# Performance work log

Measured on AMD Instinct MI355X. Metric: run time of the kernel, lower is better.

## Reference

```python
import jax, jax.numpy as jnp
import numpy as np

B, N, ND = 4096, 28, 3        # batch, nodes (2 hands x 14 joints), xyz
ED, DD = 512, 256             # encoder dim, decoder dim
H, DH = 8, 64                 # heads, dim_head (inner = 512)
EDEPTH, DDEPTH = 2, 1
EMLP, DMLP = 4 * ED, 4 * DD
NM = 14                       # num_masked = int(0.5 * 28)


def _ln(x, s, b):
    m = jnp.mean(x, -1, keepdims=True)
    v = jnp.var(x, -1, keepdims=True)
    return (x - m) * jax.lax.rsqrt(v + 1e-5) * s + b


def _transformer(x, a, ln1_s, ln1_b, Wqkv, Wo, bo, ln2_s, ln2_b, W1, b1, W2, b2):
    # pre-norm transformer; adjacency a [b,n,n] enters as an additive attention bias
    b, n, _ = x.shape
    scale = DH ** -0.5
    for i in range(ln1_s.shape[0]):
        h = _ln(x, ln1_s[i], ln1_b[i])
        q, k, v = jnp.split(h @ Wqkv[i], 3, axis=-1)
        q = q.reshape(b, n, H, DH).transpose(0, 2, 1, 3)
        k = k.reshape(b, n, H, DH).transpose(0, 2, 1, 3)
        v = v.reshape(b, n, H, DH).transpose(0, 2, 1, 3)
        dots = jnp.einsum('bhid,bhjd->bhij', q, k) * scale + a[:, None]
        attn = jax.nn.softmax(dots, axis=-1)
        o = jnp.einsum('bhij,bhjd->bhid', attn, v).transpose(0, 2, 1, 3).reshape(b, n, H * DH)
        x = x + o @ Wo[i] + bo[i]
        h2 = _ln(x, ln2_s[i], ln2_b[i])
        x = x + jax.nn.gelu(h2 @ W1[i] + b1[i]) @ W2[i] + b2[i]
    return x


def setup_inputs() -> dict:
    key = jax.random.key(0)
    ks = iter(jax.random.split(key, 40))
    nrm = lambda shp, s=0.02: jax.random.normal(next(ks), shp, dtype=jnp.float32) * s
    x = jax.random.normal(next(ks), (B, N, ND), dtype=jnp.float32)
    a = jax.random.uniform(next(ks), (B, N, N), dtype=jnp.float32)
    perm = jnp.argsort(jax.random.uniform(next(ks), (B, N)), axis=-1).astype(jnp.int32)
    masked_indices, unmasked_indices = perm[:, :NM], perm[:, NM:]
    inp = dict(x=x, a=a, masked_indices=masked_indices, unmasked_indices=unmasked_indices)
    inp.update(
        W_emb=nrm((ND, ED)), b_emb=jnp.zeros((ED,), jnp.float32), pos_emb=nrm((N, ED), 0.02),
        e_ln1_s=jnp.ones((EDEPTH, ED)), e_ln1_b=jnp.zeros((EDEPTH, ED)),
        e_Wqkv=nrm((EDEPTH, ED, 3 * H * DH)), e_Wo=nrm((EDEPTH, H * DH, ED)), e_bo=jnp.zeros((EDEPTH, ED)),
        e_ln2_s=jnp.ones((EDEPTH, ED)), e_ln2_b=jnp.zeros((EDEPTH, ED)),
        e_W1=nrm((EDEPTH, ED, EMLP)), e_b1=jnp.zeros((EDEPTH, EMLP)),
        e_W2=nrm((EDEPTH, EMLP, ED)), e_b2=jnp.zeros((EDEPTH, ED)),
        enc2dec_W=nrm((ED, DD)), enc2dec_b=jnp.zeros((DD,), jnp.float32),
        mask_token=nrm((DD,), 1.0), dec_pos_emb=nrm((N, DD), 0.02),
        d_ln1_s=jnp.ones((DDEPTH, DD)), d_ln1_b=jnp.zeros((DDEPTH, DD)),
        d_Wqkv=nrm((DDEPTH, DD, 3 * H * DH)), d_Wo=nrm((DDEPTH, H * DH, DD)), d_bo=jnp.zeros((DDEPTH, DD)),
        d_ln2_s=jnp.ones((DDEPTH, DD)), d_ln2_b=jnp.zeros((DDEPTH, DD)),
        d_W1=nrm((DDEPTH, DD, DMLP)), d_b1=jnp.zeros((DDEPTH, DMLP)),
        d_W2=nrm((DDEPTH, DMLP, DD)), d_b2=jnp.zeros((DDEPTH, DD)),
        pred_W=nrm((DD, ND)), pred_b=jnp.zeros((ND,), jnp.float32),
    )
    return inp


def reference(x, a, masked_indices, unmasked_indices,
              W_emb, b_emb, pos_emb,
              e_ln1_s, e_ln1_b, e_Wqkv, e_Wo, e_bo, e_ln2_s, e_ln2_b, e_W1, e_b1, e_W2, e_b2,
              enc2dec_W, enc2dec_b, mask_token, dec_pos_emb,
              d_ln1_s, d_ln1_b, d_Wqkv, d_Wo, d_bo, d_ln2_s, d_ln2_b, d_W1, d_b1, d_W2, d_b2,
              pred_W, pred_b):
    # node embedding (1x1 conv over nodes == per-node linear) + positional embedding
    tokens = x @ W_emb + b_emb + pos_emb                                   # [B,N,ED]
    unm_tok = jnp.take_along_axis(tokens, unmasked_indices[:, :, None], axis=1)  # [B,N-NM,ED]
    masked_nodes = jnp.take_along_axis(x, masked_indices[:, :, None], axis=1)    # [B,NM,ND]
    # batched adjacency slicing (replaces the per-sample python loop in torch)
    unmasked_a = jax.vmap(lambda ai, ii: ai[ii[:, None], ii[None, :]])(a, unmasked_indices)
    enc = _transformer(unm_tok, unmasked_a,
                       e_ln1_s, e_ln1_b, e_Wqkv, e_Wo, e_bo, e_ln2_s, e_ln2_b, e_W1, e_b1, e_W2, e_b2)
    dec_tok = enc @ enc2dec_W + enc2dec_b                                  # [B,N-NM,DD]
    mask_toks = mask_token + dec_pos_emb[masked_indices]                   # [B,NM,DD]
    # NOTE: faithful to original: unmasked pos-emb tokens are computed but NOT used in the cat
    decoder_tokens = jnp.concatenate([mask_toks, dec_tok], axis=1)         # [B,N,DD]
    decoded = _transformer(decoder_tokens, a,
                           d_ln1_s, d_ln1_b, d_Wqkv, d_Wo, d_bo, d_ln2_s, d_ln2_b, d_W1, d_b1, d_W2, d_b2)
    mt = jnp.take_along_axis(decoded, masked_indices[:, :, None], axis=1)  # [B,NM,DD]
    masked_pred = mt @ pred_W + pred_b                                     # [B,NM,ND]
    recon_loss = jnp.mean((masked_pred - masked_nodes) ** 2)
    return (decoder_tokens, masked_nodes, masked_indices, masked_pred, recon_loss)
```

## Files before the change

### kernel.cpp

```cpp
#include <hip/hip_runtime.h>
#include <math.h>

#define B_TOT 4096
#define N_SEQ 28
#define NDIM 3
#define ED 512
#define DD 256
#define NH 8
#define DHD 64
#define EMLP 2048
#define DMLP 1024
#define NM 14
#define NU 14

typedef __attribute__((ext_vector_type(8))) short short8;
typedef __attribute__((ext_vector_type(4))) float f32x4;
typedef unsigned short ushort_t;
typedef unsigned int uint_t;

__device__ __forceinline__ float gelu_f(float x) {
    float t = 0.7978845608028654f * (x + 0.044715f * x * x * x);
    float e = __expf(2.0f * t);
    float th = 1.0f - 2.0f / (e + 1.0f);
    return 0.5f * x * (1.0f + th);
}
__device__ __forceinline__ ushort_t f2bf(float f) {
    union { float f; uint_t u; } c; c.f = f;
    uint_t u = c.u;
    return (ushort_t)((u + 0x7FFFu + ((u >> 16) & 1u)) >> 16);
}
__device__ __forceinline__ float bf2f(ushort_t h) {
    union { uint_t u; float f; } c; c.u = ((uint_t)h) << 16;
    return c.f;
}
__device__ __forceinline__ float bf_lo(uint_t u) {
    union { uint_t u; float f; } c; c.u = u << 16;
    return c.f;
}
__device__ __forceinline__ float bf_hi(uint_t u) {
    union { uint_t u; float f; } c; c.u = u & 0xFFFF0000u;
    return c.f;
}
__device__ __forceinline__ void gl_lds16(const ushort_t* g, ushort_t* l) {
    __builtin_amdgcn_global_load_lds(
        (const __attribute__((address_space(1))) unsigned int*)g,
        (__attribute__((address_space(3))) unsigned int*)l, 16, 0, 0);
}

__global__ void k_zero(float* p) { p[threadIdx.x] = 0.0f; }
__global__ void k_final(const float* acc, float* out) {
    out[0] = acc[0] * (1.0f / (float)(B_TOT * NM * NDIM));
}

__global__ void k_wconv(const float* __restrict__ W, ushort_t* __restrict__ Wt, int K, int N) {
    __shared__ float tile[32][33];
    int n0 = blockIdx.x * 32, k0 = blockIdx.y * 32;
    int tr = threadIdx.x >> 5, tc = threadIdx.x & 31;
#pragma unroll
    for (int i = 0; i < 4; ++i)
        tile[tr + i * 8][tc] = W[(size_t)(k0 + tr + i * 8) * N + n0 + tc];
    __syncthreads();
#pragma unroll
    for (int i = 0; i < 4; ++i)
        Wt[(size_t)(n0 + tr + i * 8) * K + k0 + tc] = f2bf(tile[tc][tr + i * 8]);
}

__global__ void k_embed(const float* __restrict__ x, const float* __restrict__ a,
                        const int* __restrict__ mi, const int* __restrict__ ui,
                        const float* __restrict__ W_emb, const float* __restrict__ b_emb,
                        const float* __restrict__ pos_emb,
                        ushort_t* __restrict__ X, float* __restrict__ ua,
                        float* __restrict__ out_mn, float* __restrict__ out_midx,
                        int base) {
    int s = blockIdx.x;
    int g = base + s;
    int t = threadIdx.x;
    for (int i = 0; i < NU; ++i) {
        int u = ui[g * NU + i];
        float x0 = x[((size_t)g * N_SEQ + u) * NDIM + 0];
        float x1 = x[((size_t)g * N_SEQ + u) * NDIM + 1];
        float x2 = x[((size_t)g * N_SEQ + u) * NDIM + 2];
        for (int d = t; d < ED; d += 256) {
            X[((size_t)s * NU + i) * ED + d] = f2bf(
                x0 * W_emb[d] + x1 * W_emb[ED + d] + x2 * W_emb[2 * ED + d]
                + b_emb[d] + pos_emb[(size_t)u * ED + d]);
        }
    }
    for (int idx = t; idx < NU * NU; idx += 256) {
        int i = idx / NU, j = idx % NU;
        int uii = ui[g * NU + i], ujj = ui[g * NU + j];
        ua[(size_t)s * NU * NU + idx] = a[(size_t)g * N_SEQ * N_SEQ + (size_t)uii * N_SEQ + ujj];
    }
    for (int idx = t; idx < NM * NDIM; idx += 256) {
        int i = idx / NDIM, c = idx % NDIM;
        int m = mi[g * NM + i];
        out_mn[((size_t)g * NM + i) * NDIM + c] = x[((size_t)g * N_SEQ + m) * NDIM + c];
    }
    for (int i = t; i < NM; i += 256) {
        out_midx[(size_t)g * NM + i] = (float)mi[g * NM + i];
    }
}

template <int D>
__global__ void k_ln(const ushort_t* __restrict__ in, ushort_t* __restrict__ out,
                     const float* __restrict__ sc, const float* __restrict__ bi, int M) {
    int wave = threadIdx.x >> 6;
    int lane = threadIdx.x & 63;
    int row = blockIdx.x * 4 + wave;
    if (row >= M) return;
    constexpr int PL = D / 64;
    const ushort_t* rp = in + (size_t)row * D + lane * PL;
    uint_t u[PL / 2];
    if (PL == 8) *(uint4*)u = *(const uint4*)rp;
    else *(uint2*)u = *(const uint2*)rp;
    float v[PL];
    float sum = 0.f, sq = 0.f;
#pragma unroll
    for (int q = 0; q < PL / 2; ++q) {
        v[2 * q] = bf_lo(u[q]);
        v[2 * q + 1] = bf_hi(u[q]);
    }
#pragma unroll
    for (int j = 0; j < PL; ++j) { sum += v[j]; sq += v[j] * v[j]; }
#pragma unroll
    for (int o = 32; o >= 1; o >>= 1) {
        sum += __shfl_xor(sum, o);
        sq += __shfl_xor(sq, o);
    }
    float mean = sum * (1.0f / D);
    float var = sq * (1.0f / D) - mean * mean;
    float r = rsqrtf(var + 1e-5f);
    uint_t w[PL / 2];
#pragma unroll
    for (int q = 0; q < PL / 2; ++q) {
        int d = lane * PL + 2 * q;
        float a0 = (v[2 * q] - mean) * r * sc[d] + bi[d];
        float a1 = (v[2 * q + 1] - mean) * r * sc[d + 1] + bi[d + 1];
        w[q] = (uint_t)f2bf(a0) | ((uint_t)f2bf(a1) << 16);
    }
    ushort_t* op = out + (size_t)row * D + lane * PL;
    if (PL == 8) *(uint4*)op = *(uint4*)w;
    else *(uint2*)op = *(uint2*)w;
}

template <int ACT>
__global__ __launch_bounds__(256) void k_gemm_mfma(
    const ushort_t* __restrict__ A, const ushort_t* __restrict__ Wt,
    const float* __restrict__ bias, const ushort_t* __restrict__ res,
    ushort_t* __restrict__ Cout, int M, int N, int K) {
    __shared__ __align__(16) ushort_t smem[17408];
    ushort_t* As0 = smem;
    ushort_t* As1 = smem + 4096;
    ushort_t* Bs0 = smem + 8192;
    ushort_t* Bs1 = smem + 12288;

    const int t = threadIdx.x;
    const int gx = gridDim.x;
    int flat = blockIdx.y * gx + blockIdx.x;
    int nwg = gx * gridDim.y;
    int q8 = nwg >> 3, r8 = nwg & 7;
    int xcd = flat & 7, loc = flat >> 3;
    int wg = (xcd < r8 ? xcd * (q8 + 1) : r8 * (q8 + 1) + (xcd - r8) * q8) + loc;
    const int bm = wg / gx, bn = wg % gx;

    const int lane = t & 63;
    const int wave = t >> 6;
    const int wr = wave >> 1, wc = wave & 1;
    const int l15 = lane & 15;
    const int g4 = lane >> 4;
    const int kq = (g4 ^ ((l15 >> 1) & 3)) * 8;

    const int srow = wave * 32 + (lane >> 2);
    const int scol = ((lane & 3) ^ ((lane >> 3) & 3)) * 8;
    const ushort_t* Ag = A + (size_t)(bm * 128 + srow) * K + scol;
    const ushort_t* Bg = Wt + (size_t)(bn * 128 + srow) * K + scol;
    const int wb0 = (wave * 32) * 32;
    const int wb1 = (wave * 32 + 16) * 32;

    f32x4 acc[4][4] = {};
    const int nt = K >> 5;

    gl_lds16(Ag, As0 + wb0);
    gl_lds16(Ag + (size_t)16 * K, As0 + wb1);
    gl_lds16(Bg, Bs0 + wb0);
    gl_lds16(Bg + (size_t)16 * K, Bs0 + wb1);

    for (int tt = 0; tt < nt; ++tt) {
        ushort_t* Ac = (tt & 1) ? As1 : As0;
        ushort_t* Bc = (tt & 1) ? Bs1 : Bs0;
        if (tt + 1 < nt) {
            int k0 = (tt + 1) << 5;
            ushort_t* An = (tt & 1) ? As0 : As1;
            ushort_t* Bn = (tt & 1) ? Bs0 : Bs1;
            gl_lds16(Ag + k0, An + wb0);
            gl_lds16(Ag + (size_t)16 * K + k0, An + wb1);
            gl_lds16(Bg + k0, Bn + wb0);
            gl_lds16(Bg + (size_t)16 * K + k0, Bn + wb1);
            asm volatile("s_waitcnt vmcnt(4)" ::: "memory");
        } else {
            asm volatile("s_waitcnt vmcnt(0)" ::: "memory");
        }
        __builtin_amdgcn_s_barrier();
        __builtin_amdgcn_sched_barrier(0);
        short8 af[4], bfr[4];
#pragma unroll
        for (int m = 0; m < 4; ++m)
            af[m] = *(const short8*)&Ac[(wr * 64 + m * 16 + l15) * 32 + kq];
#pragma unroll
        for (int n = 0; n < 4; ++n)
            bfr[n] = *(const short8*)&Bc[(wc * 64 + n * 16 + l15) * 32 + kq];
#pragma unroll
        for (int m = 0; m < 4; ++m)
#pragma unroll
            for (int n = 0; n < 4; ++n)
                acc[m][n] = __builtin_amdgcn_mfma_f32_16x16x32_bf16(af[m], bfr[n], acc[m][n], 0, 0, 0);
        __builtin_amdgcn_sched_barrier(0);
        __builtin_amdgcn_s_barrier();
    }

    ushort_t* Cs = smem;
    const int erow0 = wr * 64, ecol0 = wc * 64;
#pragma unroll
    for (int m = 0; m < 4; ++m)
#pragma unroll
        for (int n = 0; n < 4; ++n)
#pragma unroll
            for (int r = 0; r < 4; ++r) {
                float v = acc[m][n][r];
                float o = __shfl_xor(v, 1);
                if (!(l15 & 1)) {
                    uint_t pk = (uint_t)f2bf(v) | ((uint_t)f2bf(o) << 16);
                    *(uint_t*)&Cs[(erow0 + m * 16 + g4 * 4 + r) * 136 + ecol0 + n * 16 + l15] = pk;
                }
            }
    __builtin_amdgcn_s_barrier();

    const int row = t >> 1, half = t & 1;
    const int grow = bm * 128 + row;
    const int gc0 = bn * 128 + half * 64;
    const ushort_t* rres = res ? res + (size_t)grow * N + gc0 : (const ushort_t*)0;
    ushort_t* gout = Cout + (size_t)grow * N + gc0;
#pragma unroll
    for (int c = 0; c < 8; ++c) {
        uint4 pv = *(const uint4*)&Cs[row * 136 + half * 64 + c * 8];
        uint_t* pw = (uint_t*)&pv;
        float vv[8];
#pragma unroll
        for (int q = 0; q < 4; ++q) { vv[2 * q] = bf_lo(pw[q]); vv[2 * q + 1] = bf_hi(pw[q]); }
        if (bias) {
#pragma unroll
            for (int j = 0; j < 8; ++j) vv[j] += bias[gc0 + c * 8 + j];
        }
        if (res) {
            uint4 rv = *(const uint4*)(rres + c * 8);
            uint_t* pr = (uint_t*)&rv;
#pragma unroll
            for (int q = 0; q < 4; ++q) { vv[2 * q] += bf_lo(pr[q]); vv[2 * q + 1] += bf_hi(pr[q]); }
        }
        if (ACT == 1) {
#pragma unroll
            for (int j = 0; j < 8; ++j) vv[j] = gelu_f(vv[j]);
        }
        uint4 ov;
        uint_t* po = (uint_t*)&ov;
#pragma unroll
        for (int q = 0; q < 4; ++q)
            po[q] = (uint_t)f2bf(vv[2 * q]) | ((uint_t)f2bf(vv[2 * q + 1]) << 16);
        *(uint4*)(gout + c * 8) = ov;
    }
}

template <int NT>
__global__ __launch_bounds__(256) void k_attn_mfma(
    const ushort_t* __restrict__ qkv, const float* __restrict__ bias,
    ushort_t* __restrict__ O) {
    constexpr int NTP = (NT + 15) & ~15;
    constexpr int MT = NTP / 16;
    constexpr int QS = 72;
    constexpr int VS = 40;
    __shared__ __align__(16) ushort_t smem[4 * NTP * QS * 2 + 4 * 64 * VS];
    ushort_t* Qs = smem;
    ushort_t* Ks = smem + 4 * NTP * QS;
    ushort_t* Vs = Ks + 4 * NTP * QS;
    ushort_t* Ps = smem;

    const int s = blockIdx.x, hg = blockIdx.y;
    const int t = threadIdx.x;
    const int wave = t >> 6, lane = t & 63;
    const int l15 = lane & 15, g4 = lane >> 4;

    const ushort_t* qb = qkv + (size_t)s * NT * 1536 + hg * 256;
    for (int c = t; c < 64 * NT; c += 256) {
        int c8 = c & 7;
        int rem = c >> 3;
        int r = rem % NT;
        int ph = rem / NT;
        int h = ph & 3, p = ph >> 2;
        uint4 v = *(const uint4*)(qb + (size_t)r * 1536 + p * 512 + h * 64 + c8 * 8);
        ushort_t* dst = (p ? Ks : Qs) + (h * NTP + r) * QS + c8 * 8;
        *(uint4*)dst = v;
    }
    const ushort_t* vrow = qkv + (size_t)s * NT * 1536 + 1024 + hg * 256;
    for (int c = t; c < 4 * 64 * (32 - NT); c += 256) {
        int p = c % (32 - NT);
        int hd = c / (32 - NT);
        Vs[hd * VS + NT + p] = 0;
    }
    for (int c = t; c < 4 * NT * 8; c += 256) {
        int c8 = c & 7;
        int r = (c >> 3) % NT;
        int h = (c >> 3) / NT;
        uint4 v = *(const uint4*)(vrow + (size_t)r * 1536 + h * 64 + c8 * 8);
        const uint_t* pv = (const uint_t*)&v;
#pragma unroll
        for (int j = 0; j < 4; ++j) {
            Vs[(h * 64 + c8 * 8 + 2 * j) * VS + r] = (ushort_t)(pv[j] & 0xFFFFu);
            Vs[(h * 64 + c8 * 8 + 2 * j + 1) * VS + r] = (ushort_t)(pv[j] >> 16);
        }
    }
    __syncthreads();

    const int h = wave;
    const ushort_t* Qh = Qs + h * NTP * QS;
    const ushort_t* Kh = Ks + h * NTP * QS;
    const ushort_t* Vh = Vs + h * 64 * VS;
    ushort_t* Ph = Ps + h * NTP * VS;

    f32x4 sacc[MT][MT] = {};
#pragma unroll
    for (int ks = 0; ks < 2; ++ks) {
        short8 qf[MT], kf[MT];
#pragma unroll
        for (int m = 0; m < MT; ++m)
            qf[m] = *(const short8*)&Qh[(m * 16 + l15) * QS + ks * 32 + g4 * 8];
#pragma unroll
        for (int n = 0; n < MT; ++n)
            kf[n] = *(const short8*)&Kh[(n * 16 + l15) * QS + ks * 32 + g4 * 8];
#pragma unroll
        for (int m = 0; m < MT; ++m)
#pragma unroll
            for (int n = 0; n < MT; ++n)
                sacc[m][n] = __builtin_amdgcn_mfma_f32_16x16x32_bf16(qf[m], kf[n], sacc[m][n], 0, 0, 0);
    }

    const float* bp = bias + (size_t)s * NT * NT;
    float prv[MT][MT][4];
#pragma unroll
    for (int m = 0; m < MT; ++m) {
#pragma unroll
        for (int r = 0; r < 4; ++r) {
            int i = m * 16 + g4 * 4 + r;
            float sv[MT];
#pragma unroll
            for (int n = 0; n < MT; ++n) {
                int j = n * 16 + l15;
                sv[n] = (i < NT && j < NT) ? sacc[m][n][r] * 0.125f + bp[i * NT + j] : -1e30f;
            }
            float mx = sv[0];
            if (MT > 1) mx = fmaxf(mx, sv[MT - 1]);
#pragma unroll
            for (int o = 1; o < 16; o <<= 1) mx = fmaxf(mx, __shfl_xor(mx, o));
            float sum = 0.f;
#pragma unroll
            for (int n = 0; n < MT; ++n) {
                float e = (sv[n] > -1e29f) ? __expf(sv[n] - mx) : 0.f;
                prv[m][n][r] = e;
                sum += e;
            }
#pragma unroll
            for (int o = 1; o < 16; o <<= 1) sum += __shfl_xor(sum, o);
            float rs = sum > 0.f ? 1.0f / sum : 0.f;
#pragma unroll
            for (int n = 0; n < MT; ++n) prv[m][n][r] *= rs;
        }
    }
    __syncthreads();

    if (NTP == 16) {
        for (int z = lane; z < 16 * 8; z += 64) {
            int i = z >> 3, jw = z & 7;
            *(uint_t*)&Ph[i * VS + 16 + jw * 2] = 0;
        }
    }
#pragma unroll
    for (int m = 0; m < MT; ++m)
#pragma unroll
        for (int n = 0; n < MT; ++n)
#pragma unroll
            for (int r = 0; r < 4; ++r)
                Ph[(m * 16 + g4 * 4 + r) * VS + n * 16 + l15] = f2bf(prv[m][n][r]);
    __syncthreads();

    f32x4 oacc[MT][4] = {};
    {
        short8 pf[MT], vf[4];
#pragma unroll
        for (int m = 0; m < MT; ++m)
            pf[m] = *(const short8*)&Ph[(m * 16 + l15) * VS + g4 * 8];
#pragma unroll
        for (int nd = 0; nd < 4; ++nd)
            vf[nd] = *(const short8*)&Vh[(nd * 16 + l15) * VS + g4 * 8];
#pragma unroll
        for (int m = 0; m < MT; ++m)
#pragma unroll
            for (int nd = 0; nd < 4; ++nd)
                oacc[m][nd] = __builtin_amdgcn_mfma_f32_16x16x32_bf16(pf[m], vf[nd], oacc[m][nd], 0, 0, 0);
    }

    ushort_t* Ob = O + (size_t)s * NT * 512 + hg * 256 + h * 64;
#pragma unroll
    for (int m = 0; m < MT; ++m)
#pragma unroll
        for (int r = 0; r < 4; ++r) {
            int i = m * 16 + g4 * 4 + r;
            if (i < NT) {
#pragma unroll
                for (int nd = 0; nd < 4; ++nd)
                    Ob[(size_t)i * 512 + nd * 16 + l15] = f2bf(oacc[m][nd][r]);
            }
        }
}

__global__ void k_build_dec(const ushort_t* __restrict__ dec_tok, const float* __restrict__ mask_token,
                            const float* __restrict__ dec_pos, const int* __restrict__ mi,
                            ushort_t* __restrict__ Xd, float* __restrict__ out0, int base) {
    int s = blockIdx.x;
    int g = base + s;
    int t = threadIdx.x;
    for (int idx = t; idx < N_SEQ * DD; idx += 256) {
        int i = idx / DD, d = idx % DD;
        float v;
        if (i < NM) {
            int m = mi[g * NM + i];
            v = mask_token[d] + dec_pos[(size_t)m * DD + d];
        } else {
            v = bf2f(dec_tok[((size_t)s * NU + (i - NM)) * DD + d]);
        }
        Xd[((size_t)s * N_SEQ + i) * DD + d] = f2bf(v);
        out0[((size_t)g * N_SEQ + i) * DD + d] = v;
    }
}

__global__ void k_pred(const ushort_t* __restrict__ Xd, const int* __restrict__ mi,
                       const float* __restrict__ pW, const float* __restrict__ pb,
                       const float* __restrict__ mn, float* __restrict__ out_pred,
                       float* __restrict__ loss, int base, int Bc) {
    int tid = blockIdx.x * 256 + threadIdx.x;
    int total = Bc * NM * NDIM;
    float part = 0.f;
    if (tid < total) {
        int c = tid % NDIM;
        int r = tid / NDIM;
        int i = r % NM;
        int s = r / NM;
        int g = base + s;
        int m = mi[g * NM + i];
        const ushort_t* row = Xd + ((size_t)s * N_SEQ + m) * DD;
        float acc = pb[c];
        for (int k = 0; k < DD; ++k) acc += bf2f(row[k]) * pW[k * NDIM + c];
        out_pred[((size_t)g * NM + i) * NDIM + c] = acc;
        float d = acc - mn[((size_t)g * NM + i) * NDIM + c];
        part = d * d;
    }
    __shared__ float red[256];
    red[threadIdx.x] = part;
    __syncthreads();
    for (int o = 128; o > 0; o >>= 1) {
        if (threadIdx.x < o) red[threadIdx.x] += red[threadIdx.x + o];
        __syncthreads();
    }
    if (threadIdx.x == 0) atomicAdd(loss, red[0]);
}

extern "C" void kernel_launch(void* const* d_in, const int* in_sizes, int n_in,
                              void* d_out, int out_size, void* d_ws, size_t ws_size,
                              hipStream_t stream) {
    const float* x       = (const float*)d_in[0];
    const float* a       = (const float*)d_in[1];
    const int*   mi      = (const int*)d_in[2];
    const int*   ui      = (const int*)d_in[3];
    const float* W_emb   = (const float*)d_in[4];
    const float* b_emb   = (const float*)d_in[5];
    const float* pos_emb = (const float*)d_in[6];
    const float* e_ln1_s = (const float*)d_in[7];
    const float* e_ln1_b = (const float*)d_in[8];
    const float* e_Wqkv  = (const float*)d_in[9];
    const float* e_Wo    = (const float*)d_in[10];
    const float* e_bo    = (const float*)d_in[11];
    const float* e_ln2_s = (const float*)d_in[12];
    const float* e_ln2_b = (const float*)d_in[13];
    const float* e_W1    = (const float*)d_in[14];
    const float* e_b1    = (const float*)d_in[15];
    const float* e_W2    = (const float*)d_in[16];
    const float* e_b2    = (const float*)d_in[17];
    const float* e2d_W   = (const float*)d_in[18];
    const float* e2d_b   = (const float*)d_in[19];
    const float* mask_tok= (const float*)d_in[20];
    const float* dec_pos = (const float*)d_in[21];
    const float* d_ln1_s = (const float*)d_in[22];
    const float* d_ln1_b = (const float*)d_in[23];
    const float* d_Wqkv  = (const float*)d_in[24];
    const float* d_Wo    = (const float*)d_in[25];
    const float* d_bo    = (const float*)d_in[26];
    const float* d_ln2_s = (const float*)d_in[27];
    const float* d_ln2_b = (const float*)d_in[28];
    const float* d_W1    = (const float*)d_in[29];
    const float* d_b1    = (const float*)d_in[30];
    const float* d_W2    = (const float*)d_in[31];
    const float* d_b2    = (const float*)d_in[32];
    const float* pred_W  = (const float*)d_in[33];
    const float* pred_b  = (const float*)d_in[34];

    float* out0 = (float*)d_out;
    float* out1 = out0 + (size_t)B_TOT * N_SEQ * DD;
    float* out2 = out1 + (size_t)B_TOT * NM * NDIM;
    float* out3 = out2 + (size_t)B_TOT * NM;
    float* out4 = out3 + (size_t)B_TOT * NM * NDIM;

    char* wp = (char*)d_ws;
    size_t off = 0;
    auto alloc = [&](size_t bytes) {
        size_t o = off;
        off = (off + bytes + 255) & ~(size_t)255;
        return (void*)(wp + o);
    };
    float* loss_acc = (float*)alloc(64 * 4);
    ushort_t* wt_eqkv = (ushort_t*)alloc((size_t)2 * 1536 * 512 * 2);
    ushort_t* wt_ewo  = (ushort_t*)alloc((size_t)2 * 512 * 512 * 2);
    ushort_t* wt_ew1  = (ushort_t*)alloc((size_t)2 * 2048 * 512 * 2);
    ushort_t* wt_ew2  = (ushort_t*)alloc((size_t)2 * 512 * 2048 * 2);
    ushort_t* wt_dqkv = (ushort_t*)alloc((size_t)1536 * 256 * 2);
    ushort_t* wt_dwo  = (ushort_t*)alloc((size_t)256 * 512 * 2);
    ushort_t* wt_dw1  = (ushort_t*)alloc((size_t)1024 * 256 * 2);
    ushort_t* wt_dw2  = (ushort_t*)alloc((size_t)256 * 1024 * 2);
    ushort_t* wt_e2d  = (ushort_t*)alloc((size_t)256 * 512 * 2);
    size_t fixed_bytes = off;

    const size_t per_seq = 2 * (7168 + 3584 + 7168 + 43008 + 14336) + 4 * 196;
    int Bc = B_TOT;
    while (Bc > 64 && fixed_bytes + (size_t)Bc * per_seq + 8192 > ws_size) Bc >>= 1;

    ushort_t* Xbuf   = (ushort_t*)alloc((size_t)Bc * 7168 * 2);
    ushort_t* Dbuf   = (ushort_t*)alloc((size_t)Bc * 3584 * 2);
    float*    uabuf  = (float*)alloc((size_t)Bc * 196 * 4);
    ushort_t* Hbuf   = (ushort_t*)alloc((size_t)Bc * 7168 * 2);
    ushort_t* QKVbuf = (ushort_t*)alloc((size_t)Bc * 43008 * 2);
    ushort_t* Obuf   = (ushort_t*)alloc((size_t)Bc * 14336 * 2);

    k_zero<<<1, 64, 0, stream>>>(loss_acc);

    for (int l = 0; l < 2; ++l) {
        k_wconv<<<dim3(1536 / 32, 512 / 32), 256, 0, stream>>>(e_Wqkv + (size_t)l * 512 * 1536, wt_eqkv + (size_t)l * 1536 * 512, 512, 1536);
        k_wconv<<<dim3(512 / 32, 512 / 32), 256, 0, stream>>>(e_Wo + (size_t)l * 512 * 512, wt_ewo + (size_t)l * 512 * 512, 512, 512);
        k_wconv<<<dim3(2048 / 32, 512 / 32), 256, 0, stream>>>(e_W1 + (size_t)l * 512 * 2048, wt_ew1 + (size_t)l * 2048 * 512, 512, 2048);
        k_wconv<<<dim3(512 / 32, 2048 / 32), 256, 0, stream>>>(e_W2 + (size_t)l * 2048 * 512, wt_ew2 + (size_t)l * 512 * 2048, 2048, 512);
    }
    k_wconv<<<dim3(1536 / 32, 256 / 32), 256, 0, stream>>>(d_Wqkv, wt_dqkv, 256, 1536);
    k_wconv<<<dim3(256 / 32, 512 / 32), 256, 0, stream>>>(d_Wo, wt_dwo, 512, 256);
    k_wconv<<<dim3(1024 / 32, 256 / 32), 256, 0, stream>>>(d_W1, wt_dw1, 256, 1024);
    k_wconv<<<dim3(256 / 32, 1024 / 32), 256, 0, stream>>>(d_W2, wt_dw2, 1024, 256);
    k_wconv<<<dim3(256 / 32, 512 / 32), 256, 0, stream>>>(e2d_W, wt_e2d, 512, 256);

    const int nchunk = B_TOT / Bc;
    for (int c = 0; c < nchunk; ++c) {
        int base = c * Bc;
        int M = Bc * NU;
        int Md = Bc * N_SEQ;

        k_embed<<<Bc, 256, 0, stream>>>(x, a, mi, ui, W_emb, b_emb, pos_emb,
                                        Xbuf, uabuf, out1, out2, base);
        for (int l = 0; l < 2; ++l) {
            k_ln<ED><<<M / 4, 256, 0, stream>>>(Xbuf, Hbuf, e_ln1_s + l * ED, e_ln1_b + l * ED, M);
            k_gemm_mfma<0><<<dim3(1536 / 128, M / 128), 256, 0, stream>>>(
                Hbuf, wt_eqkv + (size_t)l * 1536 * 512, nullptr, nullptr, QKVbuf, M, 1536, ED);
            k_attn_mfma<NU><<<dim3(Bc, 2), 256, 0, stream>>>(QKVbuf, uabuf, Obuf);
            k_gemm_mfma<0><<<dim3(ED / 128, M / 128), 256, 0, stream>>>(
                Obuf, wt_ewo + (size_t)l * 512 * 512, e_bo + l * ED, Xbuf, Xbuf, M, ED, 512);
            k_ln<ED><<<M / 4, 256, 0, stream>>>(Xbuf, Hbuf, e_ln2_s + l * ED, e_ln2_b + l * ED, M);
            k_gemm_mfma<1><<<dim3(EMLP / 128, M / 128), 256, 0, stream>>>(
                Hbuf, wt_ew1 + (size_t)l * 2048 * 512, e_b1 + l * EMLP, nullptr, QKVbuf, M, EMLP, ED);
            k_gemm_mfma<0><<<dim3(ED / 128, M / 128), 256, 0, stream>>>(
                QKVbuf, wt_ew2 + (size_t)l * 512 * 2048, e_b2 + l * ED, Xbuf, Xbuf, M, ED, EMLP);
        }
        k_gemm_mfma<0><<<dim3(DD / 128, M / 128), 256, 0, stream>>>(
            Xbuf, wt_e2d, e2d_b, nullptr, Dbuf, M, DD, ED);
        k_build_dec<<<Bc, 256, 0, stream>>>(Dbuf, mask_tok, dec_pos, mi, Xbuf, out0, base);
        k_ln<DD><<<Md / 4, 256, 0, stream>>>(Xbuf, Hbuf, d_ln1_s, d_ln1_b, Md);
        k_gemm_mfma<0><<<dim3(1536 / 128, Md / 128), 256, 0, stream>>>(
            Hbuf, wt_dqkv, nullptr, nullptr, QKVbuf, Md, 1536, DD);
        k_attn_mfma<N_SEQ><<<dim3(Bc, 2), 256, 0, stream>>>(QKVbuf, a + (size_t)base * N_SEQ * N_SEQ, Obuf);
        k_gemm_mfma<0><<<dim3(DD / 128, Md / 128), 256, 0, stream>>>(
            Obuf, wt_dwo, d_bo, Xbuf, Xbuf, Md, DD, 512);
        k_ln<DD><<<Md / 4, 256, 0, stream>>>(Xbuf, Hbuf, d_ln2_s, d_ln2_b, Md);
        k_gemm_mfma<1><<<dim3(DMLP / 128, Md / 128), 256, 0, stream>>>(
            Hbuf, wt_dw1, d_b1, nullptr, QKVbuf, Md, DMLP, DD);
        k_gemm_mfma<0><<<dim3(DD / 128, Md / 128), 256, 0, stream>>>(
            QKVbuf, wt_dw2, d_b2, Xbuf, Xbuf, Md, DD, DMLP);
        int tot = Bc * NM * NDIM;
        k_pred<<<(tot + 255) / 256, 256, 0, stream>>>(
            Xbuf, mi, pred_W, pred_b, out1, out3, loss_acc, base, Bc);
    }
    k_final<<<1, 1, 0, stream>>>(loss_acc, out4);
}
```

Baseline: 2.803 ms.

## Triple-buffer GEMM LDS staging with one barrier per k-tile

Switches the bf16 MFMA GEMM from double to triple buffering of its A/B tiles in shared memory, issuing loads two k-tiles ahead. The trailing per-iteration barrier is removed because the third buffer prevents overwriting a tile still being read. The goal is to hide more global-load latency and cut synchronisation. In exchange, LDS use per block grows (about 48KB), which may lower occupancy.

```diff
diff --git a/kernel.cpp b/kernel.cpp
--- a/kernel.cpp
+++ b/kernel.cpp
@@ -148,11 +148,7 @@
     const ushort_t* __restrict__ A, const ushort_t* __restrict__ Wt,
     const float* __restrict__ bias, const ushort_t* __restrict__ res,
     ushort_t* __restrict__ Cout, int M, int N, int K) {
-    __shared__ __align__(16) ushort_t smem[17408];
-    ushort_t* As0 = smem;
-    ushort_t* As1 = smem + 4096;
-    ushort_t* Bs0 = smem + 8192;
-    ushort_t* Bs1 = smem + 12288;
+    __shared__ __align__(16) ushort_t smem[24576];
 
     const int t = threadIdx.x;
     const int gx = gridDim.x;
@@ -180,28 +176,33 @@
     f32x4 acc[4][4] = {};
     const int nt = K >> 5;
 
-    gl_lds16(Ag, As0 + wb0);
-    gl_lds16(Ag + (size_t)16 * K, As0 + wb1);
-    gl_lds16(Bg, Bs0 + wb0);
-    gl_lds16(Bg + (size_t)16 * K, Bs0 + wb1);
-
+#define STAGE(tile, idx)                                          \
+    do {                                                          \
+        int k0_ = (tile) << 5;                                    \
+        ushort_t* Ab_ = smem + (idx) * 8192;                      \
+        ushort_t* Bb_ = Ab_ + 4096;                               \
+        gl_lds16(Ag + k0_, Ab_ + wb0);                            \
+        gl_lds16(Ag + (size_t)16 * K + k0_, Ab_ + wb1);           \
+        gl_lds16(Bg + k0_, Bb_ + wb0);                            \
+        gl_lds16(Bg + (size_t)16 * K + k0_, Bb_ + wb1);           \
+    } while (0)
+
+    STAGE(0, 0);
+    STAGE(1, 1);
+
+    int cur = 0;
     for (int tt = 0; tt < nt; ++tt) {
-        ushort_t* Ac = (tt & 1) ? As1 : As0;
-        ushort_t* Bc = (tt & 1) ? Bs1 : Bs0;
-        if (tt + 1 < nt) {
-            int k0 = (tt + 1) << 5;
-            ushort_t* An = (tt & 1) ? As0 : As1;
-            ushort_t* Bn = (tt & 1) ? Bs0 : Bs1;
-            gl_lds16(Ag + k0, An + wb0);
-            gl_lds16(Ag + (size_t)16 * K + k0, An + wb1);
-            gl_lds16(Bg + k0, Bn + wb0);
-            gl_lds16(Bg + (size_t)16 * K + k0, Bn + wb1);
-            asm volatile("s_waitcnt vmcnt(4)" ::: "memory");
-        } else {
-            asm volatile("s_waitcnt vmcnt(0)" ::: "memory");
-        }
+        if (tt + 1 < nt) asm volatile("s_waitcnt vmcnt(4)" ::: "memory");
+        else             asm volatile("s_waitcnt vmcnt(0)" ::: "memory");
         __builtin_amdgcn_s_barrier();
         __builtin_amdgcn_sched_barrier(0);
+        if (tt + 2 < nt) {
+            int nidx = cur + 2; if (nidx >= 3) nidx -= 3;
+            STAGE(tt + 2, nidx);
+        }
+        __builtin_amdgcn_sched_barrier(0);
+        const ushort_t* Ac = smem + cur * 8192;
+        const ushort_t* Bc = Ac + 4096;
         short8 af[4], bfr[4];
 #pragma unroll
         for (int m = 0; m < 4; ++m)
@@ -214,9 +215,12 @@
 #pragma unroll
             for (int n = 0; n < 4; ++n)
                 acc[m][n] = __builtin_amdgcn_mfma_f32_16x16x32_bf16(af[m], bfr[n], acc[m][n], 0, 0, 0);
-        __builtin_amdgcn_sched_barrier(0);
-        __builtin_amdgcn_s_barrier();
-    }
+        if (++cur == 3) cur = 0;
+    }
+#undef STAGE
+
+    __builtin_amdgcn_sched_barrier(0);
+    __builtin_amdgcn_s_barrier();
 
     ushort_t* Cs = smem;
     const int erow0 = wr * 64, ecol0 = wc * 64;
```

New measurement: 2.731 ms. -2.6%, faster.
